# Kernel optimization log

Measured on AMD Instinct MI355X. Metric: run time of the kernel, lower is better.

The kernel has to match this reference:

```python
import jax, jax.numpy as jnp
import numpy as np

D = 512
MOMENTUM = 0.99
NEG_INF = -1.0e9


def setup_inputs() -> dict:
    key = jax.random.key(0)
    ks = jax.random.split(key, 16)
    B, Lq, Lk = 16, 1024, 1024
    s = 0.02
    inp = {
        "uncond_q": jax.random.normal(ks[0], (B, D), jnp.float32),
        "q": jax.random.normal(ks[1], (B, Lq, D), jnp.float32),
        "k": jax.random.normal(ks[2], (B, Lk, D), jnp.float32),
        "v": jax.random.normal(ks[3], (B, Lk, D), jnp.float32),
        "src_key_padding_mask": jax.random.randint(ks[4], (B, Lk), 0, 2) > 0,
        "fallback_score": jnp.zeros((1,), jnp.float32),
        # parameters (torch Linear: y = x @ W.T + b)
        "Wv": jax.random.normal(ks[5], (D, D), jnp.float32) * s,
        "bv": jnp.zeros((D,), jnp.float32),
        "Wf": jax.random.normal(ks[6], (D, D), jnp.float32) * s,
        "bf": jnp.zeros((D,), jnp.float32),
        "W1": jax.random.normal(ks[7], (D, D), jnp.float32) * s,
        "b1": jnp.zeros((D,), jnp.float32),
        "W2": jax.random.normal(ks[8], (D // 2, D), jnp.float32) * s,
        "b2": jnp.zeros((D // 2,), jnp.float32),
        "W3": jax.random.normal(ks[9], (1, D // 2), jnp.float32) * s,
        "b3": jnp.zeros((1,), jnp.float32),
    }
    return inp


def _scorer(x, W1, b1, W2, b2, W3, b3):
    h = jax.nn.relu(x @ W1.T + b1)
    h = jax.nn.relu(h @ W2.T + b2)
    return jnp.tanh(h @ W3.T + b3)


def reference(uncond_q, q, k, v, src_key_padding_mask, fallback_score,
              Wv, bv, Wf, bf, W1, b1, W2, b2, W3, b3):
    B, Lq, _ = q.shape
    v_p = v @ Wv.T + bv                                  # [B,Lk,D]
    default_values = (uncond_q @ Wf.T + bf)[:, None, :]  # [B,1,D]

    scores = jnp.einsum('bqd,bkd->bqk', q, k) / jnp.sqrt(jnp.float32(D))

    # EMA fallback-score update (training mode), detached from grads
    bmax = jax.lax.stop_gradient(scores.max())
    bmin = jax.lax.stop_gradient(scores.min())
    fb = MOMENTUM * fallback_score[0] + (1.0 - MOMENTUM) * (bmax + bmin) / 2.0

    scores = jnp.where(src_key_padding_mask[:, None, :], NEG_INF, scores)
    fb_col = jnp.broadcast_to(fb, (B, Lq, 1))
    scores = jnp.concatenate([scores, fb_col], axis=-1)   # [B,Lq,Lk+1]
    weights = jax.nn.softmax(scores, axis=-1)

    v_padded = jnp.concatenate([v_p, default_values], axis=1)  # [B,Lk+1,D]
    out = jnp.einsum('bqk,bkd->bqd', weights, v_padded)

    return (_scorer(out, W1, b1, W2, b2, W3, b3),
            _scorer(default_values, W1, b1, W2, b2, W3, b3))
```

## Files before the change

### kernel.cpp

```cpp
#include <hip/hip_runtime.h>

typedef _Float16 f16;
typedef f16  f16x8 __attribute__((ext_vector_type(8)));
typedef f16  f16x4 __attribute__((ext_vector_type(4)));
typedef __fp16 fp16x2 __attribute__((ext_vector_type(2)));
typedef float f32x4 __attribute__((ext_vector_type(4)));

__device__ __forceinline__ void gld_lds16(const f16* g, void* l) {
  __builtin_amdgcn_global_load_lds((const __attribute__((address_space(1))) void*)g,
                                   (__attribute__((address_space(3))) void*)l,
                                   16, 0, 0);
}

__device__ __forceinline__ f16x8 pack8(float4 a, float4 b) {
  union { f16x8 v; fp16x2 h[4]; } u;
  u.h[0] = __builtin_amdgcn_cvt_pkrtz(a.x, a.y);
  u.h[1] = __builtin_amdgcn_cvt_pkrtz(a.z, a.w);
  u.h[2] = __builtin_amdgcn_cvt_pkrtz(b.x, b.y);
  u.h[3] = __builtin_amdgcn_cvt_pkrtz(b.z, b.w);
  return u.v;
}

enum { EPI_SCORES = 0, EPI_RELU = 2, EPI_OUT = 3, EPI_BIASR = 4 };

template<int EPI, bool XMAP>
__global__ __launch_bounds__(256)
void gemm_bt(const f16* __restrict__ A, const f16* __restrict__ B, void* __restrict__ C,
             int lda, int ldb, int ldc, int K,
             long long sA, long long sB, long long sC,
             const float* __restrict__ bias, float scale,
             const float* __restrict__ wfb, const float* __restrict__ dvv,
             int nx, int nbz)
{
  __shared__ __align__(16) f16 As[4][128][32];
  __shared__ __align__(16) f16 Bs[4][128][32];
  const int tid  = threadIdx.x;
  const int lane = tid & 63;
  const int w    = tid >> 6;
  const int wm   = w >> 1, wn = w & 1;

  const int lin = blockIdx.x;
  int bz, bj;
  if constexpr (XMAP) {
    const int xcd = lin & 7, rest = lin >> 3;
    const int grp = rest / nbz;
    bj = rest - grp * nbz;
    bz = xcd + (grp << 3);
  } else {
    bz = lin / nbz; bj = lin - bz * nbz;
  }
  const int m0 = (bj / nx) * 128, n0 = (bj % nx) * 128;
  const f16* Ab = A + (size_t)bz * sA + (size_t)m0 * lda;
  const f16* Bb = B + (size_t)bz * sB + (size_t)n0 * ldb;

  f32x4 acc[4][4] = {};
  const int nsteps = K >> 5;

#define STAGE(bufb, ks)                                                              \
  {                                                                                  \
    const int k0_ = (ks) << 5;                                                       \
    _Pragma("unroll")                                                                \
    for (int i = 0; i < 2; ++i) {                                                    \
      const int ci = i * 256 + tid;                                                  \
      const int r  = ci >> 2;                                                        \
      const int sg = (ci & 3) ^ ((r >> 1) & 3);                                      \
      gld_lds16(Ab + (size_t)r * lda + k0_ + sg * 8,                                 \
                (char*)As + (bufb) + (size_t)(i * 256 + w * 64) * 16);               \
      gld_lds16(Bb + (size_t)r * ldb + k0_ + sg * 8,                                 \
                (char*)Bs + (bufb) + (size_t)(i * 256 + w * 64) * 16);               \
    }                                                                                \
  }

  STAGE(0, 0)
  if (1 < nsteps) STAGE(8192, 1)
  if (2 < nsteps) STAGE(16384, 2)

  const int elemoff = (((lane >> 4) ^ ((lane >> 1) & 3)) << 3);

  int cur = 0;
  for (int t = 0; t < nsteps; ++t) {
    if (t + 2 < nsteps)      asm volatile("s_waitcnt vmcnt(8)" ::: "memory");
    else if (t + 1 < nsteps) asm volatile("s_waitcnt vmcnt(4)" ::: "memory");
    else                     asm volatile("s_waitcnt vmcnt(0)" ::: "memory");
    __builtin_amdgcn_s_barrier();
    __builtin_amdgcn_sched_barrier(0);
    if (t + 3 < nsteps) STAGE(((cur + 3) & 3) * 8192, t + 3)
    f16x8 af[4], bfr[4];
#pragma unroll
    for (int m = 0; m < 4; ++m)
      af[m] = *(const f16x8*)&As[cur][wm * 64 + m * 16 + (lane & 15)][elemoff];
#pragma unroll
    for (int n = 0; n < 4; ++n)
      bfr[n] = *(const f16x8*)&Bs[cur][wn * 64 + n * 16 + (lane & 15)][elemoff];
    __builtin_amdgcn_s_setprio(1);
#pragma unroll
    for (int m = 0; m < 4; ++m)
#pragma unroll
      for (int n = 0; n < 4; ++n)
        acc[m][n] = __builtin_amdgcn_mfma_f32_16x16x32_f16(af[m], bfr[n], acc[m][n], 0, 0, 0);
    __builtin_amdgcn_s_setprio(0);
    cur = (cur + 1) & 3;
  }
#undef STAGE

  const int col_l = lane & 15;
  const int row_l = (lane >> 4) << 2;

  {
    f16* Ch = (f16*)C + (size_t)bz * sC + (size_t)m0 * ldc + n0;
#pragma unroll
    for (int m = 0; m < 4; ++m)
#pragma unroll
      for (int n = 0; n < 4; ++n)
#pragma unroll
        for (int r = 0; r < 4; ++r) {
          const int rr = wm * 64 + m * 16 + row_l + r;
          const int cc = wn * 64 + n * 16 + col_l;
          float val = acc[m][n][r];
          if constexpr (EPI == EPI_RELU) { val += bias[n0 + cc]; val = fmaxf(val, 0.0f); }
          if constexpr (EPI == EPI_BIASR) val += bias[m0 + rr];
          if constexpr (EPI == EPI_OUT)
            val += wfb[bz * 1024 + m0 + rr] * dvv[bz * 512 + n0 + cc];
          Ch[(size_t)rr * ldc + cc] = (f16)val;
        }
  }
  (void)scale;
}

__global__ __launch_bounds__(512, 2)
void gemm256_scores(const float* __restrict__ A, const float* __restrict__ B, f16* __restrict__ C,
                    float scale, float* __restrict__ mmarr)
{
  __shared__ __align__(16) f16 As[3][256][32];
  __shared__ __align__(16) f16 Bs[3][256][32];
  __shared__ float redm[8], redn[8];
  const int tid  = threadIdx.x;
  const int lane = tid & 63;
  const int w    = tid >> 6;
  const int wm   = w >> 2, wn = w & 3;
  const int lin  = blockIdx.x;
  const int xcd = lin & 7, rest = lin >> 3;
  const int bj  = rest & 15;
  const int bz  = xcd + ((rest >> 4) << 3);
  const int m0 = (bj >> 2) * 256, n0 = (bj & 3) * 256;
  const float* Ab = A + (size_t)bz * 524288 + (size_t)m0 * 512;
  const float* Bb = B + (size_t)bz * 524288 + (size_t)n0 * 512;

  const int r0  = tid >> 2;
  const int sg0 = (tid & 3) ^ ((r0 >> 1) & 3);
  const size_t offG = (size_t)r0 * 512 + sg0 * 8;
  f16* const dstA0 = (f16*)As + (size_t)tid * 8;
  f16* const dstB0 = (f16*)Bs + (size_t)tid * 8;

  f32x4 acc[8][4] = {};

#pragma unroll
  for (int s = 0; s < 2; ++s) {
    const int k0 = s << 5;
    float4 a0 = *(const float4*)(Ab + offG + k0);
    float4 a1 = *(const float4*)(Ab + offG + k0 + 4);
    float4 a2 = *(const float4*)(Ab + offG + k0 + 65536);
    float4 a3 = *(const float4*)(Ab + offG + k0 + 65540);
    float4 b0 = *(const float4*)(Bb + offG + k0);
    float4 b1 = *(const float4*)(Bb + offG + k0 + 4);
    float4 b2 = *(const float4*)(Bb + offG + k0 + 65536);
    float4 b3 = *(const float4*)(Bb + offG + k0 + 65540);
    *(f16x8*)(dstA0 + s * 8192)        = pack8(a0, a1);
    *(f16x8*)(dstA0 + s * 8192 + 4096) = pack8(a2, a3);
    *(f16x8*)(dstB0 + s * 8192)        = pack8(b0, b1);
    *(f16x8*)(dstB0 + s * 8192 + 4096) = pack8(b2, b3);
  }
  float4 ha0, ha1, ha2, ha3, hb0, hb1, hb2, hb3;
  {
    const int k0 = 2 << 5;
    ha0 = *(const float4*)(Ab + offG + k0);
    ha1 = *(const float4*)(Ab + offG + k0 + 4);
    ha2 = *(const float4*)(Ab + offG + k0 + 65536);
    ha3 = *(const float4*)(Ab + offG + k0 + 65540);
    hb0 = *(const float4*)(Bb + offG + k0);
    hb1 = *(const float4*)(Bb + offG + k0 + 4);
    hb2 = *(const float4*)(Bb + offG + k0 + 65536);
    hb3 = *(const float4*)(Bb + offG + k0 + 65540);
  }
  __syncthreads();

  const int fr = lane & 15;
  const int elemoff = (((lane >> 4) ^ ((lane >> 1) & 3)) << 3);

  int cur = 0;
  for (int t = 0; t < 16; ++t) {
    f16x8 af[8], bfr[4];
#pragma unroll
    for (int m = 0; m < 8; ++m)
      af[m] = *(const f16x8*)&As[cur][wm * 128 + m * 16 + fr][elemoff];
#pragma unroll
    for (int n = 0; n < 4; ++n)
      bfr[n] = *(const f16x8*)&Bs[cur][wn * 64 + n * 16 + fr][elemoff];
    if (t + 2 < 16) {
      int wb = cur + 2; if (wb >= 3) wb -= 3;
      *(f16x8*)(dstA0 + wb * 8192)        = pack8(ha0, ha1);
      *(f16x8*)(dstA0 + wb * 8192 + 4096) = pack8(ha2, ha3);
      *(f16x8*)(dstB0 + wb * 8192)        = pack8(hb0, hb1);
      *(f16x8*)(dstB0 + wb * 8192 + 4096) = pack8(hb2, hb3);
    }
    if (t + 3 < 16) {
      const int k0 = (t + 3) << 5;
      ha0 = *(const float4*)(Ab + offG + k0);
      ha1 = *(const float4*)(Ab + offG + k0 + 4);
      ha2 = *(const float4*)(Ab + offG + k0 + 65536);
      ha3 = *(const float4*)(Ab + offG + k0 + 65540);
      hb0 = *(const float4*)(Bb + offG + k0);
      hb1 = *(const float4*)(Bb + offG + k0 + 4);
      hb2 = *(const float4*)(Bb + offG + k0 + 65536);
      hb3 = *(const float4*)(Bb + offG + k0 + 65540);
    }
    __builtin_amdgcn_s_setprio(1);
#pragma unroll
    for (int m = 0; m < 8; ++m)
#pragma unroll
      for (int n = 0; n < 4; ++n)
        acc[m][n] = __builtin_amdgcn_mfma_f32_16x16x32_f16(af[m], bfr[n], acc[m][n], 0, 0, 0);
    __builtin_amdgcn_s_setprio(0);
    asm volatile("s_waitcnt lgkmcnt(0)" ::: "memory");
    __builtin_amdgcn_sched_barrier(0);
    __builtin_amdgcn_s_barrier();
    cur = (cur + 1 == 3) ? 0 : cur + 1;
  }

  const int col_l = lane & 15;
  const int row_l = (lane >> 4) << 2;
  f16* Ch = C + (size_t)bz * 1048576 + (size_t)m0 * 1024 + n0;
  float lmax = -3.402823466e38f, lmin = 3.402823466e38f;
#pragma unroll
  for (int m = 0; m < 8; ++m)
#pragma unroll
    for (int n = 0; n < 4; ++n)
#pragma unroll
      for (int r = 0; r < 4; ++r) {
        float val = acc[m][n][r] * scale;
        lmax = fmaxf(lmax, val); lmin = fminf(lmin, val);
        Ch[(size_t)(wm * 128 + m * 16 + row_l + r) * 1024 + (wn * 64 + n * 16 + col_l)] = (f16)val;
      }
#pragma unroll
  for (int off = 32; off >= 1; off >>= 1) {
    lmax = fmaxf(lmax, __shfl_xor(lmax, off));
    lmin = fminf(lmin, __shfl_xor(lmin, off));
  }
  if (lane == 0) { redm[w] = lmax; redn[w] = lmin; }
  __syncthreads();
  if (tid == 0) {
    float gm = redm[0], gn = redn[0];
#pragma unroll
    for (int i = 1; i < 8; ++i) { gm = fmaxf(gm, redm[i]); gn = fminf(gn, redn[i]); }
    mmarr[lin] = gm; mmarr[256 + lin] = gn;
  }
}

__global__ __launch_bounds__(256)
void gemm_vpt(const f16* __restrict__ A, const float* __restrict__ B, f16* __restrict__ C,
              const float* __restrict__ bias)
{
  __shared__ __align__(16) f16 As[3][128][32];
  __shared__ __align__(16) f16 Bs[3][128][32];
  const int tid  = threadIdx.x;
  const int lane = tid & 63;
  const int w    = tid >> 6;
  const int wm   = w >> 1, wn = w & 1;
  const int lin  = blockIdx.x;
  const int xcd = lin & 7, rest = lin >> 3;
  const int grp = rest >> 5, bj = rest & 31;
  const int bz  = xcd + (grp << 3);
  const int m0 = (bj >> 3) * 128, n0 = (bj & 7) * 128;
  const f16*   Ab = A + (size_t)m0 * 512;
  const float* Bb = B + (size_t)bz * 524288 + (size_t)n0 * 512;

  const int r0  = tid >> 2;
  const int sg0 = (tid & 3) ^ ((r0 >> 1) & 3);
  const size_t offA = (size_t)r0 * 512 + sg0 * 8;
  const size_t offB = (size_t)r0 * 512 + sg0 * 8;
  f16* const dstA0 = (f16*)As + (size_t)tid * 8;
  f16* const dstB0 = (f16*)Bs + (size_t)tid * 8;

  f32x4 acc[4][4] = {};

#pragma unroll
  for (int s = 0; s < 2; ++s) {
    const int k0 = s << 5;
    f16x8  a0 = *(const f16x8*)(Ab + offA + k0);
    f16x8  a1 = *(const f16x8*)(Ab + offA + k0 + 32768);
    float4 b0 = *(const float4*)(Bb + offB + k0);
    float4 b1 = *(const float4*)(Bb + offB + k0 + 4);
    float4 b2 = *(const float4*)(Bb + offB + k0 + 32768);
    float4 b3 = *(const float4*)(Bb + offB + k0 + 32772);
    *(f16x8*)(dstA0 + s * 4096)        = a0;
    *(f16x8*)(dstA0 + s * 4096 + 2048) = a1;
    *(f16x8*)(dstB0 + s * 4096)        = pack8(b0, b1);
    *(f16x8*)(dstB0 + s * 4096 + 2048) = pack8(b2, b3);
  }
  __syncthreads();

  const int fr = lane & 15;
  const int elemoff = (((lane >> 4) ^ ((lane >> 1) & 3)) << 3);

  int cur = 0;
  for (int t = 0; t < 16; ++t) {
    f16x8  a0, a1; float4 b0, b1, b2, b3;
    if (t + 2 < 16) {
      const int k0 = (t + 2) << 5;
      a0 = *(const f16x8*)(Ab + offA + k0);
      a1 = *(const f16x8*)(Ab + offA + k0 + 32768);
      b0 = *(const float4*)(Bb + offB + k0);
      b1 = *(const float4*)(Bb + offB + k0 + 4);
      b2 = *(const float4*)(Bb + offB + k0 + 32768);
      b3 = *(const float4*)(Bb + offB + k0 + 32772);
    }
    f16x8 af[4], bfr[4];
#pragma unroll
    for (int m = 0; m < 4; ++m)
      af[m] = *(const f16x8*)&As[cur][wm * 64 + m * 16 + fr][elemoff];
#pragma unroll
    for (int n = 0; n < 4; ++n)
      bfr[n] = *(const f16x8*)&Bs[cur][wn * 64 + n * 16 + fr][elemoff];
    __builtin_amdgcn_s_setprio(1);
#pragma unroll
    for (int m = 0; m < 4; ++m)
#pragma unroll
      for (int n = 0; n < 4; ++n)
        acc[m][n] = __builtin_amdgcn_mfma_f32_16x16x32_f16(af[m], bfr[n], acc[m][n], 0, 0, 0);
    __builtin_amdgcn_s_setprio(0);
    if (t + 2 < 16) {
      int wb = cur + 2; if (wb >= 3) wb -= 3;
      *(f16x8*)(dstA0 + wb * 4096)        = a0;
      *(f16x8*)(dstA0 + wb * 4096 + 2048) = a1;
      *(f16x8*)(dstB0 + wb * 4096)        = pack8(b0, b1);
      *(f16x8*)(dstB0 + wb * 4096 + 2048) = pack8(b2, b3);
    }
    __syncthreads();
    cur = (cur + 1 == 3) ? 0 : cur + 1;
  }

  const int col_l = lane & 15;
  const int row_l = (lane >> 4) << 2;
  f16* Ch = C + (size_t)bz * 524288 + (size_t)m0 * 1024 + n0;
#pragma unroll
  for (int m = 0; m < 4; ++m)
#pragma unroll
    for (int n = 0; n < 4; ++n)
#pragma unroll
      for (int r = 0; r < 4; ++r) {
        const int rr = wm * 64 + m * 16 + row_l + r;
        const int cc = wn * 64 + n * 16 + col_l;
        Ch[(size_t)rr * 1024 + cc] = (f16)(acc[m][n][r] + bias[m0 + rr]);
      }
}

__global__ __launch_bounds__(256)
void front_k(const float* __restrict__ wv, const float* __restrict__ w1,
             const float* __restrict__ w2,
             f16* __restrict__ owv, f16* __restrict__ ow1, f16* __restrict__ ow2,
             const float* __restrict__ uq, const float* __restrict__ Wf,
             const float* __restrict__ bfv, float* __restrict__ dv,
             const unsigned char* __restrict__ mask, unsigned* __restrict__ mm)
{
  const int blk = blockIdx.x;
  if (blk < 640) {
    int i = blk * 256 + threadIdx.x;
    const float* src; f16* dst; int j;
    if (i < 65536)       { src = wv; dst = owv; j = i; }
    else if (i < 131072) { src = w1; dst = ow1; j = i - 65536; }
    else                 { src = w2; dst = ow2; j = i - 131072; }
    float4 x = *(const float4*)(src + (size_t)j * 4);
    f16x4 o = { (f16)x.x, (f16)x.y, (f16)x.z, (f16)x.w };
    *(f16x4*)(dst + (size_t)j * 4) = o;
  } else if (blk < 2688) {
    const int gw   = ((blk - 640) * 256 + threadIdx.x) >> 6;
    const int lane = threadIdx.x & 63;
    const int b = gw >> 9, j = gw & 511;
    const float* x  = uq + (size_t)b * 512;
    const float* wr = Wf + (size_t)j * 512;
    const int o = lane * 8;
    float4 x0 = *(const float4*)(x + o),  x1 = *(const float4*)(x + o + 4);
    float4 w0 = *(const float4*)(wr + o), w1v = *(const float4*)(wr + o + 4);
    float s = x0.x*w0.x + x0.y*w0.y + x0.z*w0.z + x0.w*w0.w
            + x1.x*w1v.x + x1.y*w1v.y + x1.z*w1v.z + x1.w*w1v.w;
#pragma unroll
    for (int off = 32; off >= 1; off >>= 1) s += __shfl_xor(s, off);
    if (lane == 0) dv[gw] = s + bfv[j];
  } else {
    __shared__ int redc[256];
    int c = 0;
    for (int i = threadIdx.x; i < 16384; i += 256) c += (mask[i] != 0) ? 1 : 0;
    redc[threadIdx.x] = c;
    __syncthreads();
    for (int s = 128; s > 0; s >>= 1) {
      if (threadIdx.x < s) redc[threadIdx.x] += redc[threadIdx.x + s];
      __syncthreads();
    }
    if (threadIdx.x == 0) mm[0] = (unsigned)redc[0];
  }
}

__global__ __launch_bounds__(256)
void softmax_rows(const f16* __restrict__ scores, const void* __restrict__ maskp,
                  const float* __restrict__ fallback, const float* __restrict__ mmarr,
                  const unsigned* __restrict__ mm,
                  f16* __restrict__ Wt, float* __restrict__ wfb)
{
  __shared__ float red[8];
  const int row  = blockIdx.x;
  const int b    = row >> 10;
  const int tid  = threadIdx.x;
  const int lane = tid & 63, w = tid >> 6;

  float mx0 = mmarr[tid];
  float mn0 = mmarr[256 + tid];
#pragma unroll
  for (int off = 32; off >= 1; off >>= 1) {
    mx0 = fmaxf(mx0, __shfl_xor(mx0, off));
    mn0 = fminf(mn0, __shfl_xor(mn0, off));
  }
  if (lane == 0) { red[w] = mx0; red[4 + w] = mn0; }
  __syncthreads();
  const float gmax = fmaxf(fmaxf(red[0], red[1]), fmaxf(red[2], red[3]));
  const float gmin = fminf(fminf(red[4], red[5]), fminf(red[6], red[7]));
  const float fb = 0.99f * fallback[0] + 0.005f * (gmax + gmin);
  const unsigned mode = (mm[0] > 5000u) ? 1u : 0u;
  __syncthreads();

  const f16* s = scores + (size_t)row * 1024;
  const int k0 = tid * 4;
  f16x4 sv = *(const f16x4*)(s + k0);
  float x[4];
  if (mode) {
    const unsigned char* m8 = (const unsigned char*)maskp + b * 1024 + k0;
    x[0] = m8[0] ? -1e9f : (float)sv[0];  x[1] = m8[1] ? -1e9f : (float)sv[1];
    x[2] = m8[2] ? -1e9f : (float)sv[2];  x[3] = m8[3] ? -1e9f : (float)sv[3];
  } else {
    const int* mi = (const int*)maskp + b * 1024 + k0;
    x[0] = mi[0] ? -1e9f : (float)sv[0];  x[1] = mi[1] ? -1e9f : (float)sv[1];
    x[2] = mi[2] ? -1e9f : (float)sv[2];  x[3] = mi[3] ? -1e9f : (float)sv[3];
  }
  float mx = fmaxf(fmaxf(x[0], x[1]), fmaxf(x[2], x[3]));
#pragma unroll
  for (int off = 32; off >= 1; off >>= 1) mx = fmaxf(mx, __shfl_xor(mx, off));
  if (lane == 0) red[w] = mx;
  __syncthreads();
  mx = fmaxf(fmaxf(fmaxf(red[0], red[1]), fmaxf(red[2], red[3])), fb);
  float e0 = expf(x[0] - mx), e1 = expf(x[1] - mx), e2 = expf(x[2] - mx), e3 = expf(x[3] - mx);
  float sum = (e0 + e1) + (e2 + e3);
#pragma unroll
  for (int off = 32; off >= 1; off >>= 1) sum += __shfl_xor(sum, off);
  if (lane == 0) red[4 + w] = sum;
  __syncthreads();
  float efb = expf(fb - mx);
  float Z = ((red[4] + red[5]) + (red[6] + red[7])) + efb;
  float inv = 1.0f / Z;
  f16x4 o = { (f16)(e0 * inv), (f16)(e1 * inv), (f16)(e2 * inv), (f16)(e3 * inv) };
  *(f16x4*)&Wt[(size_t)row * 1024 + k0] = o;
  if (tid == 0) wfb[row] = efb * inv;
}

template<int IN, int ACT>
__global__ __launch_bounds__(256)
void fc_wave(const float* __restrict__ X, const float* __restrict__ W,
             const float* __restrict__ bias, float* __restrict__ Y, int OutN)
{
  const int gw   = (blockIdx.x * 256 + threadIdx.x) >> 6;
  const int lane = threadIdx.x & 63;
  const int b = gw / OutN, j = gw - b * OutN;
  const float* x  = X + (size_t)b * IN;
  const float* wr = W + (size_t)j * IN;
  float s = 0.f;
  if constexpr (IN == 512) {
    const int o = lane * 8;
    float4 x0 = *(const float4*)(x + o),  x1 = *(const float4*)(x + o + 4);
    float4 w0 = *(const float4*)(wr + o), w1 = *(const float4*)(wr + o + 4);
    s = x0.x*w0.x + x0.y*w0.y + x0.z*w0.z + x0.w*w0.w
      + x1.x*w1.x + x1.y*w1.y + x1.z*w1.z + x1.w*w1.w;
  } else {
    const int o = lane * 4;
    float4 x0 = *(const float4*)(x + o);
    float4 w0 = *(const float4*)(wr + o);
    s = x0.x*w0.x + x0.y*w0.y + x0.z*w0.z + x0.w*w0.w;
  }
#pragma unroll
  for (int off = 32; off >= 1; off >>= 1) s += __shfl_xor(s, off);
  if (lane == 0) {
    float val = s + bias[ACT == 2 ? 0 : j];
    if constexpr (ACT == 1) val = fmaxf(val, 0.f);
    if constexpr (ACT == 2) val = tanhf(val);
    Y[gw] = val;
  }
}

__global__ __launch_bounds__(256)
void y_kernel(const f16* __restrict__ h2, const float* __restrict__ W3,
              const float* __restrict__ b3, float* __restrict__ outp)
{
  int row = blockIdx.x * 16 + (threadIdx.x >> 4);
  int l   = threadIdx.x & 15;
  const f16* h = h2 + (size_t)row * 256 + l * 16;
  float s = 0.f;
#pragma unroll
  for (int j = 0; j < 16; ++j) s += (float)h[j] * W3[l * 16 + j];
#pragma unroll
  for (int off = 1; off < 16; off <<= 1) s += __shfl_xor(s, off);
  if (l == 0) outp[row] = tanhf(s + b3[0]);
}

extern "C" void kernel_launch(void* const* d_in, const int* in_sizes, int n_in,
                              void* d_out, int out_size, void* d_ws, size_t ws_size,
                              hipStream_t stream) {
  const float* uq       = (const float*)d_in[0];
  const float* q        = (const float*)d_in[1];
  const float* kk       = (const float*)d_in[2];
  const float* v        = (const float*)d_in[3];
  const void*  mask     = d_in[4];
  const float* fallback = (const float*)d_in[5];
  const float* Wv = (const float*)d_in[6];
  const float* bv = (const float*)d_in[7];
  const float* Wf = (const float*)d_in[8];
  const float* bf = (const float*)d_in[9];
  const float* W1 = (const float*)d_in[10];
  const float* b1 = (const float*)d_in[11];
  const float* W2 = (const float*)d_in[12];
  const float* b2 = (const float*)d_in[13];
  const float* W3 = (const float*)d_in[14];
  const float* b3 = (const float*)d_in[15];
  float* outp = (float*)d_out;

  char* ws = (char*)d_ws;
  const size_t MB = 1ull << 20;
  f16*  scores = (f16*)ws;
  f16*  h1b  = (f16*)ws;
  f16*  h2b  = (f16*)(ws + 16 * MB);
  f16*  vpt  = (f16*)(ws + 32 * MB);
  f16*  outb = (f16*)(ws + 48 * MB);
  f16*  wts  = (f16*)(ws + 64 * MB);
  char* cst  = ws + 112 * MB;
  f16*  Wv16 = (f16*)(cst);
  f16*  W116 = (f16*)(cst + 512 * 1024);
  f16*  W216 = (f16*)(cst + 1024 * 1024);
  float* dv   = (float*)(cst + 1280 * 1024);
  float* wfb  = (float*)(cst + 1312 * 1024);
  float* h1d  = (float*)(cst + 1376 * 1024);
  float* h2d  = (float*)(cst + 1408 * 1024);
  unsigned* mm = (unsigned*)(cst + 1424 * 1024);
  float* mmarr = (float*)(cst + 1432 * 1024);

  front_k<<<2689, 256, 0, stream>>>(Wv, W1, W2, Wv16, W116, W216,
                                    uq, Wf, bf, dv,
                                    (const unsigned char*)mask, mm);

  gemm256_scores<<<256, 512, 0, stream>>>(q, kk, scores, 0.04419417382415922f, mmarr);

  softmax_rows<<<16384, 256, 0, stream>>>(scores, mask, fallback, mmarr, mm, wts, wfb);

  gemm_vpt<<<512, 256, 0, stream>>>(Wv16, v, vpt, bv);

  gemm_bt<EPI_OUT, true><<<512, 256, 0, stream>>>(
      wts, vpt, outb, 1024, 1024, 512, 1024,
      1048576LL, 524288LL, 524288LL,
      nullptr, 1.f, wfb, dv, 4, 32);

  gemm_bt<EPI_RELU, false><<<512, 256, 0, stream>>>(
      outb, W116, h1b, 512, 512, 512, 512, 0LL, 0LL, 0LL,
      b1, 1.f, nullptr, nullptr, 4, 512);

  gemm_bt<EPI_RELU, false><<<256, 256, 0, stream>>>(
      h1b, W216, h2b, 512, 512, 256, 512, 0LL, 0LL, 0LL,
      b2, 1.f, nullptr, nullptr, 2, 256);

  y_kernel<<<1024, 256, 0, stream>>>(h2b, W3, b3, outp);

  fc_wave<512, 1><<<2048, 256, 0, stream>>>(dv, W1, b1, h1d, 512);
  fc_wave<512, 1><<<1024, 256, 0, stream>>>(h1d, W2, b2, h2d, 256);
  fc_wave<256, 2><<<4, 256, 0, stream>>>(h2d, W3, b3, outp + 16384, 1);

  (void)in_sizes; (void)n_in; (void)out_size; (void)ws_size;
}
```

Measured before the change: 160.8 us.

## Halve scores GEMM N-tile to 256x128 and deepen gemm_vpt load prefetch

The scores GEMM tile shrinks from 256x256 to 256x128, which doubles the grid from 256 to 512 blocks so all CUs have work. The min/max partial array and the softmax reduction are widened to match. gemm_vpt now prefetches global data one extra stage ahead into registers, writes to LDS before the MFMAs, and replaces __syncthreads with an explicit waitcnt plus barrier. The smaller tile cuts reuse per block and raises total global traffic for q.

```diff
diff --git a/kernel.cpp b/kernel.cpp
--- a/kernel.cpp
+++ b/kernel.cpp
@@ -132,7 +132,7 @@
                     float scale, float* __restrict__ mmarr)
 {
   __shared__ __align__(16) f16 As[3][256][32];
-  __shared__ __align__(16) f16 Bs[3][256][32];
+  __shared__ __align__(16) f16 Bs[3][128][32];
   __shared__ float redm[8], redn[8];
   const int tid  = threadIdx.x;
   const int lane = tid & 63;
@@ -140,47 +140,43 @@
   const int wm   = w >> 2, wn = w & 3;
   const int lin  = blockIdx.x;
   const int xcd = lin & 7, rest = lin >> 3;
-  const int bj  = rest & 15;
-  const int bz  = xcd + ((rest >> 4) << 3);
-  const int m0 = (bj >> 2) * 256, n0 = (bj & 3) * 256;
+  const int bj  = rest & 31;
+  const int bz  = xcd + ((rest >> 5) << 3);
+  const int m0 = (bj >> 3) * 256, n0 = (bj & 7) * 128;
   const float* Ab = A + (size_t)bz * 524288 + (size_t)m0 * 512;
   const float* Bb = B + (size_t)bz * 524288 + (size_t)n0 * 512;
 
   const int r0  = tid >> 2;
   const int sg0 = (tid & 3) ^ ((r0 >> 1) & 3);
-  const size_t offG = (size_t)r0 * 512 + sg0 * 8;
+  const size_t offGA = (size_t)r0 * 512 + sg0 * 8;
+  const size_t offGB = offGA;
   f16* const dstA0 = (f16*)As + (size_t)tid * 8;
   f16* const dstB0 = (f16*)Bs + (size_t)tid * 8;
 
-  f32x4 acc[8][4] = {};
+  f32x4 acc[8][2] = {};
 
 #pragma unroll
   for (int s = 0; s < 2; ++s) {
     const int k0 = s << 5;
-    float4 a0 = *(const float4*)(Ab + offG + k0);
-    float4 a1 = *(const float4*)(Ab + offG + k0 + 4);
-    float4 a2 = *(const float4*)(Ab + offG + k0 + 65536);
-    float4 a3 = *(const float4*)(Ab + offG + k0 + 65540);
-    float4 b0 = *(const float4*)(Bb + offG + k0);
-    float4 b1 = *(const float4*)(Bb + offG + k0 + 4);
-    float4 b2 = *(const float4*)(Bb + offG + k0 + 65536);
-    float4 b3 = *(const float4*)(Bb + offG + k0 + 65540);
+    float4 a0 = *(const float4*)(Ab + offGA + k0);
+    float4 a1 = *(const float4*)(Ab + offGA + k0 + 4);
+    float4 a2 = *(const float4*)(Ab + offGA + k0 + 65536);
+    float4 a3 = *(const float4*)(Ab + offGA + k0 + 65540);
+    float4 b0 = *(const float4*)(Bb + offGB + k0);
+    float4 b1 = *(const float4*)(Bb + offGB + k0 + 4);
     *(f16x8*)(dstA0 + s * 8192)        = pack8(a0, a1);
     *(f16x8*)(dstA0 + s * 8192 + 4096) = pack8(a2, a3);
-    *(f16x8*)(dstB0 + s * 8192)        = pack8(b0, b1);
-    *(f16x8*)(dstB0 + s * 8192 + 4096) = pack8(b2, b3);
-  }
-  float4 ha0, ha1, ha2, ha3, hb0, hb1, hb2, hb3;
+    *(f16x8*)(dstB0 + s * 4096)        = pack8(b0, b1);
+  }
+  float4 ha0, ha1, ha2, ha3, hb0, hb1;
   {
     const int k0 = 2 << 5;
-    ha0 = *(const float4*)(Ab + offG + k0);
-    ha1 = *(const float4*)(Ab + offG + k0 + 4);
-    ha2 = *(const float4*)(Ab + offG + k0 + 65536);
-    ha3 = *(const float4*)(Ab + offG + k0 + 65540);
-    hb0 = *(const float4*)(Bb + offG + k0);
-    hb1 = *(const float4*)(Bb + offG + k0 + 4);
-    hb2 = *(const float4*)(Bb + offG + k0 + 65536);
-    hb3 = *(const float4*)(Bb + offG + k0 + 65540);
+    ha0 = *(const float4*)(Ab + offGA + k0);
+    ha1 = *(const float4*)(Ab + offGA + k0 + 4);
+    ha2 = *(const float4*)(Ab + offGA + k0 + 65536);
+    ha3 = *(const float4*)(Ab + offGA + k0 + 65540);
+    hb0 = *(const float4*)(Bb + offGB + k0);
+    hb1 = *(const float4*)(Bb + offGB + k0 + 4);
   }
   __syncthreads();
 
@@ -189,36 +185,33 @@
 
   int cur = 0;
   for (int t = 0; t < 16; ++t) {
-    f16x8 af[8], bfr[4];
+    f16x8 af[8], bfr[2];
 #pragma unroll
     for (int m = 0; m < 8; ++m)
       af[m] = *(const f16x8*)&As[cur][wm * 128 + m * 16 + fr][elemoff];
 #pragma unroll
-    for (int n = 0; n < 4; ++n)
-      bfr[n] = *(const f16x8*)&Bs[cur][wn * 64 + n * 16 + fr][elemoff];
+    for (int n = 0; n < 2; ++n)
+      bfr[n] = *(const f16x8*)&Bs[cur][wn * 32 + n * 16 + fr][elemoff];
     if (t + 2 < 16) {
       int wb = cur + 2; if (wb >= 3) wb -= 3;
       *(f16x8*)(dstA0 + wb * 8192)        = pack8(ha0, ha1);
       *(f16x8*)(dstA0 + wb * 8192 + 4096) = pack8(ha2, ha3);
-      *(f16x8*)(dstB0 + wb * 8192)        = pack8(hb0, hb1);
-      *(f16x8*)(dstB0 + wb * 8192 + 4096) = pack8(hb2, hb3);
+      *(f16x8*)(dstB0 + wb * 4096)        = pack8(hb0, hb1);
     }
     if (t + 3 < 16) {
       const int k0 = (t + 3) << 5;
-      ha0 = *(const float4*)(Ab + offG + k0);
-      ha1 = *(const float4*)(Ab + offG + k0 + 4);
-      ha2 = *(const float4*)(Ab + offG + k0 + 65536);
-      ha3 = *(const float4*)(Ab + offG + k0 + 65540);
-      hb0 = *(const float4*)(Bb + offG + k0);
-      hb1 = *(const float4*)(Bb + offG + k0 + 4);
-      hb2 = *(const float4*)(Bb + offG + k0 + 65536);
-      hb3 = *(const float4*)(Bb + offG + k0 + 65540);
+      ha0 = *(const float4*)(Ab + offGA + k0);
+      ha1 = *(const float4*)(Ab + offGA + k0 + 4);
+      ha2 = *(const float4*)(Ab + offGA + k0 + 65536);
+      ha3 = *(const float4*)(Ab + offGA + k0 + 65540);
+      hb0 = *(const float4*)(Bb + offGB + k0);
+      hb1 = *(const float4*)(Bb + offGB + k0 + 4);
     }
     __builtin_amdgcn_s_setprio(1);
 #pragma unroll
     for (int m = 0; m < 8; ++m)
 #pragma unroll
-      for (int n = 0; n < 4; ++n)
+      for (int n = 0; n < 2; ++n)
         acc[m][n] = __builtin_amdgcn_mfma_f32_16x16x32_f16(af[m], bfr[n], acc[m][n], 0, 0, 0);
     __builtin_amdgcn_s_setprio(0);
     asm volatile("s_waitcnt lgkmcnt(0)" ::: "memory");
@@ -234,12 +227,12 @@
 #pragma unroll
   for (int m = 0; m < 8; ++m)
 #pragma unroll
-    for (int n = 0; n < 4; ++n)
+    for (int n = 0; n < 2; ++n)
 #pragma unroll
       for (int r = 0; r < 4; ++r) {
         float val = acc[m][n][r] * scale;
         lmax = fmaxf(lmax, val); lmin = fminf(lmin, val);
-        Ch[(size_t)(wm * 128 + m * 16 + row_l + r) * 1024 + (wn * 64 + n * 16 + col_l)] = (f16)val;
+        Ch[(size_t)(wm * 128 + m * 16 + row_l + r) * 1024 + (wn * 32 + n * 16 + col_l)] = (f16)val;
       }
 #pragma unroll
   for (int off = 32; off >= 1; off >>= 1) {
@@ -252,7 +245,7 @@
     float gm = redm[0], gn = redn[0];
 #pragma unroll
     for (int i = 1; i < 8; ++i) { gm = fmaxf(gm, redm[i]); gn = fminf(gn, redn[i]); }
-    mmarr[lin] = gm; mmarr[256 + lin] = gn;
+    mmarr[lin] = gm; mmarr[512 + lin] = gn;
   }
 }
 
@@ -297,6 +290,16 @@
     *(f16x8*)(dstB0 + s * 4096)        = pack8(b0, b1);
     *(f16x8*)(dstB0 + s * 4096 + 2048) = pack8(b2, b3);
   }
+  f16x8  hA0, hA1; float4 hB0, hB1, hB2, hB3;
+  {
+    const int k0 = 2 << 5;
+    hA0 = *(const f16x8*)(Ab + offA + k0);
+    hA1 = *(const f16x8*)(Ab + offA + k0 + 32768);
+    hB0 = *(const float4*)(Bb + offB + k0);
+    hB1 = *(const float4*)(Bb + offB + k0 + 4);
+    hB2 = *(const float4*)(Bb + offB + k0 + 32768);
+    hB3 = *(const float4*)(Bb + offB + k0 + 32772);
+  }
   __syncthreads();
 
   const int fr = lane & 15;
@@ -304,16 +307,6 @@
 
   int cur = 0;
   for (int t = 0; t < 16; ++t) {
-    f16x8  a0, a1; float4 b0, b1, b2, b3;
-    if (t + 2 < 16) {
-      const int k0 = (t + 2) << 5;
-      a0 = *(const f16x8*)(Ab + offA + k0);
-      a1 = *(const f16x8*)(Ab + offA + k0 + 32768);
-      b0 = *(const float4*)(Bb + offB + k0);
-      b1 = *(const float4*)(Bb + offB + k0 + 4);
-      b2 = *(const float4*)(Bb + offB + k0 + 32768);
-      b3 = *(const float4*)(Bb + offB + k0 + 32772);
-    }
     f16x8 af[4], bfr[4];
 #pragma unroll
     for (int m = 0; m < 4; ++m)
@@ -321,6 +314,22 @@
 #pragma unroll
     for (int n = 0; n < 4; ++n)
       bfr[n] = *(const f16x8*)&Bs[cur][wn * 64 + n * 16 + fr][elemoff];
+    if (t + 2 < 16) {
+      int wb = cur + 2; if (wb >= 3) wb -= 3;
+      *(f16x8*)(dstA0 + wb * 4096)        = hA0;
+      *(f16x8*)(dstA0 + wb * 4096 + 2048) = hA1;
+      *(f16x8*)(dstB0 + wb * 4096)        = pack8(hB0, hB1);
+      *(f16x8*)(dstB0 + wb * 4096 + 2048) = pack8(hB2, hB3);
+    }
+    if (t + 3 < 16) {
+      const int k0 = (t + 3) << 5;
+      hA0 = *(const f16x8*)(Ab + offA + k0);
+      hA1 = *(const f16x8*)(Ab + offA + k0 + 32768);
+      hB0 = *(const float4*)(Bb + offB + k0);
+      hB1 = *(const float4*)(Bb + offB + k0 + 4);
+      hB2 = *(const float4*)(Bb + offB + k0 + 32768);
+      hB3 = *(const float4*)(Bb + offB + k0 + 32772);
+    }
     __builtin_amdgcn_s_setprio(1);
 #pragma unroll
     for (int m = 0; m < 4; ++m)
@@ -328,14 +337,9 @@
       for (int n = 0; n < 4; ++n)
         acc[m][n] = __builtin_amdgcn_mfma_f32_16x16x32_f16(af[m], bfr[n], acc[m][n], 0, 0, 0);
     __builtin_amdgcn_s_setprio(0);
-    if (t + 2 < 16) {
-      int wb = cur + 2; if (wb >= 3) wb -= 3;
-      *(f16x8*)(dstA0 + wb * 4096)        = a0;
-      *(f16x8*)(dstA0 + wb * 4096 + 2048) = a1;
-      *(f16x8*)(dstB0 + wb * 4096)        = pack8(b0, b1);
-      *(f16x8*)(dstB0 + wb * 4096 + 2048) = pack8(b2, b3);
-    }
-    __syncthreads();
+    asm volatile("s_waitcnt lgkmcnt(0)" ::: "memory");
+    __builtin_amdgcn_sched_barrier(0);
+    __builtin_amdgcn_s_barrier();
     cur = (cur + 1 == 3) ? 0 : cur + 1;
   }
 
@@ -412,8 +416,8 @@
   const int tid  = threadIdx.x;
   const int lane = tid & 63, w = tid >> 6;
 
-  float mx0 = mmarr[tid];
-  float mn0 = mmarr[256 + tid];
+  float mx0 = fmaxf(mmarr[tid], mmarr[256 + tid]);
+  float mn0 = fminf(mmarr[512 + tid], mmarr[768 + tid]);
 #pragma unroll
   for (int off = 32; off >= 1; off >>= 1) {
     mx0 = fmaxf(mx0, __shfl_xor(mx0, off));
@@ -552,7 +556,7 @@
                                     uq, Wf, bf, dv,
                                     (const unsigned char*)mask, mm);
 
-  gemm256_scores<<<256, 512, 0, stream>>>(q, kk, scores, 0.04419417382415922f, mmarr);
+  gemm256_scores<<<512, 512, 0, stream>>>(q, kk, scores, 0.04419417382415922f, mmarr);
 
   softmax_rows<<<16384, 256, 0, stream>>>(scores, mask, fallback, mmarr, mm, wts, wfb);
 
```

Result: slower. 175.7 us (+9.3%).
